# Performance work log

Measured on AMD Instinct MI355X. Metric: run time of the kernel, lower is better.

The kernel has to match this reference:

```python
import jax, jax.numpy as jnp
import numpy as np

NB = 8          # num_bins
HID = 128       # hidden channels of coupling ResidualNet
TB = 3.0        # tail_bound
MINB = 1e-3     # min bin width / height
MIND = 1e-3     # min derivative
DCONST = float(np.log(np.exp(1.0 - MIND) - 1.0))  # softplus(DCONST)+MIND == 1
LU_EPS = 1e-3


def rqs_inverse(x, uw, uh, ud):
    """Inverse monotonic rational-quadratic spline with linear tails (nflows math).
    x: [B,F]; uw,uh broadcastable to [B,F,NB]; ud broadcastable to [B,F,NB-1]."""
    K = NB
    uw = jnp.broadcast_to(uw, x.shape + (K,))
    uh = jnp.broadcast_to(uh, x.shape + (K,))
    ud = jnp.broadcast_to(ud, x.shape + (K - 1,))
    ud = jnp.pad(ud, [(0, 0)] * x.ndim + [(1, 1)], constant_values=DCONST)  # boundary derivs = 1
    inside = (x >= -TB) & (x <= TB)
    xi = jnp.clip(x, -TB, TB)

    def knots(u):
        v = MINB + (1.0 - MINB * K) * jax.nn.softmax(u, -1)
        c = jnp.concatenate([jnp.zeros(x.shape + (1,), x.dtype), jnp.cumsum(v, -1)], -1)
        c = 2.0 * TB * c - TB
        c = c.at[..., 0].set(-TB).at[..., -1].set(TB)
        return c, c[..., 1:] - c[..., :-1]

    cw, w = knots(uw)   # x-knots / bin widths
    ch, h = knots(uh)   # y-knots / bin heights
    d = MIND + jax.nn.softplus(ud)  # [B,F,K+1] knot derivatives

    # searchsorted on cumheights (inverse direction)
    locs = ch.at[..., -1].add(1e-6)
    idx = jnp.clip(jnp.sum((xi[..., None] >= locs).astype(jnp.int32), -1) - 1, 0, K - 1)[..., None]
    g = lambda a: jnp.take_along_axis(a, idx, -1)[..., 0]
    in_cw, in_w, in_ch, in_h = g(cw), g(w), g(ch), g(h)
    delta = in_h / in_w
    d0 = g(d)
    d1 = jnp.take_along_axis(d, idx + 1, -1)[..., 0]

    t = xi - in_ch
    s = d0 + d1 - 2.0 * delta
    a = t * s + in_h * (delta - d0)
    b = in_h * d0 - t * s
    c = -delta * t
    root = (2.0 * c) / (-b - jnp.sqrt(b * b - 4.0 * a * c))
    out = root * in_w + in_cw
    tm = root * (1.0 - root)
    den = delta + s * tm
    dnum = delta ** 2 * (d1 * root ** 2 + 2.0 * delta * tm + d0 * (1.0 - root) ** 2)
    ld = -(jnp.log(dnum) - 2.0 * jnp.log(den))
    return jnp.where(inside, out, x), jnp.where(inside, ld, 0.0)


def resnet(x, Wi, bi, Wb, bb, Wo, bo):
    # nflows ResidualNet: initial linear, 2 pre-activation residual blocks, final linear
    t = x @ Wi + bi
    for j in range(2):
        r = jax.nn.relu(t) @ Wb[2 * j] + bb[2 * j]
        r = jax.nn.relu(r) @ Wb[2 * j + 1] + bb[2 * j + 1]
        t = t + r
    return t @ Wo + bo


def coupling_inverse(z, Wi, bi, Wb, bb, Wo, bo, uw_u, uh_u, ud_u):
    # alternating mask: even dims = identity split, odd dims = transform split
    ident, trans = z[:, 0::2], z[:, 1::2]
    # unconditional spline on identity features is inverted FIRST, then feeds the net
    ident, ld_u = rqs_inverse(ident, uw_u, uh_u, ud_u)
    B, F = trans.shape
    p = resnet(ident, Wi, bi, Wb, bb, Wo, bo).reshape(B, F, 3 * NB - 1)
    scale = 1.0 / np.sqrt(HID)  # nflows divides widths/heights by sqrt(hidden_features)
    trans, ld_t = rqs_inverse(trans, p[..., :NB] * scale, p[..., NB:2 * NB] * scale, p[..., 2 * NB:])
    out = jnp.stack([ident, trans], -1).reshape(B, -1)
    return out, jnp.sum(ld_u, -1) + jnp.sum(ld_t, -1)


def log_prob(x, loc, log_scale, Wi, bi, Wb, bb, Wo, bo, uw_u, uh_u, ud_u,
             lu_lower, lu_upper, lu_ud, lu_b, perms):
    N, T, D = x.shape
    z = x.reshape(-1, D)
    lq = jnp.zeros((z.shape[0],), x.dtype)
    for i in (2, 1, 0):  # flows = [C0,LU0,C1,LU1,C2,LU2]; invert in reverse order
        # LULinearPermute.inverse: permute, then y = L(Ux) + b, logdet = sum log diag(U)
        zp = z[:, perms[i]]
        diag = jax.nn.softplus(lu_ud[i]) + LU_EPS
        U = jnp.triu(lu_upper[i], 1) + jnp.diag(diag)
        L = jnp.tril(lu_lower[i], -1) + jnp.eye(D, dtype=x.dtype)
        z = (zp @ U.T) @ L.T + lu_b[i]
        lq = lq + jnp.sum(jnp.log(diag))
        z, ld = coupling_inverse(z, Wi[i], bi[i], Wb[i], bb[i], Wo[i], bo[i],
                                 uw_u[i], uh_u[i], ud_u[i])
        lq = lq + ld
    # DiagGaussian base log-prob
    lq = lq - 0.5 * D * jnp.log(2.0 * jnp.pi) \
            - jnp.sum(log_scale + 0.5 * ((z - loc) / jnp.exp(log_scale)) ** 2, -1)
    return lq.reshape(N, T)


def setup_inputs():
    key = jax.random.key(0)
    ks = jax.random.split(key, 16)
    N, T, D, F = 8, 512, 550, 275
    OUT = F * (3 * NB - 1)
    s = 0.1
    return {
        "x": jax.random.normal(ks[0], (N, T, D), jnp.float32),
        "loc": 0.1 * jax.random.normal(ks[1], (D,), jnp.float32),
        "log_scale": jnp.zeros((D,), jnp.float32),
        "Wi": s * jax.random.normal(ks[2], (3, F, HID), jnp.float32),
        "bi": jnp.zeros((3, HID), jnp.float32),
        "Wb": s * jax.random.normal(ks[3], (3, 4, HID, HID), jnp.float32),
        "bb": jnp.zeros((3, 4, HID), jnp.float32),
        "Wo": 0.01 * jax.random.normal(ks[4], (3, HID, OUT), jnp.float32),
        "bo": 0.01 * jax.random.normal(ks[5], (3, OUT), jnp.float32),
        "uw_u": jax.random.uniform(ks[6], (3, F, NB), jnp.float32),
        "uh_u": jax.random.uniform(ks[7], (3, F, NB), jnp.float32),
        "ud_u": jax.random.uniform(ks[8], (3, F, NB - 1), jnp.float32),
        "lu_lower": 0.05 * jax.random.normal(ks[9], (3, D, D), jnp.float32),
        "lu_upper": 0.05 * jax.random.normal(ks[10], (3, D, D), jnp.float32),
        "lu_ud": jnp.full((3, D), DCONST, jnp.float32),
        "lu_b": jnp.zeros((3, D), jnp.float32),
        "perms": jnp.stack([jax.random.permutation(ks[11 + i], D) for i in range(3)]).astype(jnp.int32),
    }


def reference(x, loc, log_scale, Wi, bi, Wb, bb, Wo, bo, uw_u, uh_u, ud_u,
              lu_lower, lu_upper, lu_ud, lu_b, perms):
    # log_prob(x).reshape(N, T); calculate_likelihood would just apply exp/nan->0/clamp on top.
    return log_prob(x, loc, log_scale, Wi, bi, Wb, bb, Wo, bo, uw_u, uh_u, ud_u,
                    lu_lower, lu_upper, lu_ud, lu_b, perms)
```

## Files before the change

kernel.cpp:

```cpp
#include <hip/hip_runtime.h>


#define D_DIM 550
#define D_PAD 576
#define N_PAD_A 640
#define F_DIM 275
#define F_PAD 320
#define FP_HALF 288
#define HID_DIM 128
#define OUT_DIM 6325
#define OUT_PAD 6400
#define FT_PAD 276
#define WO24_ROWS (FT_PAD*24)
#define WO_GX (WO24_ROWS/48)
#define B_ROWS 4096
#define NBINS 8
#define TB_C 3.0f
#define MINB_C 0.001f
#define MIND_C 0.001f
#define DCONST_C 0.53974233f
#define LUEPS_C 0.001f
#define RSQRT_HID 0.08838834764831845f

typedef unsigned short ushort_t;
typedef __attribute__((ext_vector_type(8))) short short8;
typedef __attribute__((ext_vector_type(8))) unsigned short ushort8;
typedef __attribute__((ext_vector_type(4))) float f32x4;

__device__ __forceinline__ ushort_t f2bf(float f){
    union{float f; unsigned u;} v; v.f = f;
    unsigned r = v.u + 0x7fffu + ((v.u>>16)&1u);
    return (ushort_t)(r>>16);
}
__device__ __forceinline__ float bf2f(ushort_t h){
    union{unsigned u; float f;} v; v.u = ((unsigned)h)<<16;
    return v.f;
}
__device__ __forceinline__ float softplusf(float x){
    return fmaxf(x, 0.f) + __logf(1.f + __expf(-fabsf(x)));
}

__device__ __forceinline__ void knots_from_u(const float* u, float* c, float* w){
    float m = u[0];
#pragma unroll
    for(int k=1;k<NBINS;k++) m = fmaxf(m, u[k]);
    float e[NBINS]; float s = 0.f;
#pragma unroll
    for(int k=0;k<NBINS;k++){ e[k] = __expf(u[k]-m); s += e[k]; }
    float inv = 1.f/s;
    float cum = 0.f;
    c[0] = -TB_C;
#pragma unroll
    for(int k=0;k<NBINS;k++){
        float v = MINB_C + (1.f - MINB_C*(float)NBINS)*e[k]*inv;
        cum += v;
        c[k+1] = 2.f*TB_C*cum - TB_C;
    }
    c[NBINS] = TB_C;
#pragma unroll
    for(int k=0;k<NBINS;k++) w[k] = c[k+1]-c[k];
}

__device__ __forceinline__ void rqs_inv(float x,
                                        const float* cw, const float* w,
                                        const float* ch, const float* h,
                                        const float* d,
                                        float& out, float& ld){
    bool inside = (x >= -TB_C) && (x <= TB_C);
    float xi = fminf(fmaxf(x, -TB_C), TB_C);
    int idx = 0;
#pragma unroll
    for(int j=1;j<NBINS;j++) idx += (xi >= ch[j]) ? 1 : 0;
    float icw=cw[0], iw=w[0], ich=ch[0], ih=h[0], d0=d[0], d1=d[1];
#pragma unroll
    for(int j=1;j<NBINS;j++){
        if(idx==j){ icw=cw[j]; iw=w[j]; ich=ch[j]; ih=h[j]; d0=d[j]; d1=d[j+1]; }
    }
    float delta = ih/iw;
    float t  = xi - ich;
    float s  = d0 + d1 - 2.f*delta;
    float a  = t*s + ih*(delta - d0);
    float b  = ih*d0 - t*s;
    float c  = -delta*t;
    float disc = b*b - 4.f*a*c;
    float root = 2.f*c / (-b - sqrtf(fmaxf(disc, 0.f)));
    float o  = root*iw + icw;
    float tm = root*(1.f-root);
    float den  = delta + s*tm;
    float dnum = delta*delta*(d1*root*root + 2.f*delta*tm + d0*(1.f-root)*(1.f-root));
    float l = 2.f*__logf(den) - __logf(dnum);
    out = inside ? o : x;
    ld  = inside ? l : 0.f;
}

__global__ __launch_bounds__(256)
void fat_setup(const float* __restrict__ uw_u, const float* __restrict__ uh_u,
               const float* __restrict__ ud_u, float* __restrict__ knots,
               const float* __restrict__ lu_ud, float* __restrict__ logdiag,
               const float* __restrict__ bo, float* __restrict__ bo2,
               const float* __restrict__ x, ushort_t* __restrict__ xb,
               const float* __restrict__ lower, ushort_t* __restrict__ Lmb,
               float* __restrict__ lq, float* __restrict__ zbias,
               ushort_t* __restrict__ zOddT, ushort_t* __restrict__ Wo2){
    __shared__ float sm[4];
    int b = blockIdx.x, tid = threadIdx.x;
    if(b < 4){
        int g = b*256 + tid;
        if(g >= 3*F_DIM) return;
        float* kb = knots + (size_t)g*43;
        float c[9], w[8];
        knots_from_u(uw_u + (size_t)g*8, c, w);
#pragma unroll
        for(int k=0;k<9;k++) kb[k]=c[k];
#pragma unroll
        for(int k=0;k<8;k++) kb[9+k]=w[k];
        knots_from_u(uh_u + (size_t)g*8, c, w);
#pragma unroll
        for(int k=0;k<9;k++) kb[17+k]=c[k];
#pragma unroll
        for(int k=0;k<8;k++) kb[26+k]=w[k];
        float dend = MIND_C + softplusf(DCONST_C);
        kb[34]=dend; kb[42]=dend;
        const float* ud = ud_u + (size_t)g*7;
#pragma unroll
        for(int k=0;k<7;k++) kb[35+k] = MIND_C + softplusf(ud[k]);
    } else if(b < 5){
        float s = 0.f;
        for(int k=tid; k<3*D_DIM; k+=256) s += __logf(softplusf(lu_ud[k]) + LUEPS_C);
#pragma unroll
        for(int o=32;o>0;o>>=1) s += __shfl_down(s, o);
        if((tid&63)==0) sm[tid>>6]=s;
        __syncthreads();
        if(tid==0) logdiag[0] = sm[0]+sm[1]+sm[2]+sm[3];
    } else if(b < 80){
        int idx = (b-5)*256 + tid;
        if(idx >= 3*OUT_DIM) return;
        int l = idx/OUT_DIM, n = idx%OUT_DIM;
        int f = n/23, j = n - 23*f;
        bo2[(size_t)l*WO24_ROWS + f*24 + j] = bo[idx];
    } else if(b < 9296){
        int idx = (b-80)*256 + tid;
        if(idx >= B_ROWS*D_PAD) return;
        int r = idx / D_PAD, c = idx - r*D_PAD;
        float v = (r<B_ROWS && c<D_DIM) ? x[(size_t)r*D_DIM+c] : 0.f;
        xb[idx] = f2bf(v);
    } else if(b < 14246){
        int lb = b - 9296;
        int l = lb/1650;
        int rem = lb - l*1650;
        int j = rem/3;
        int xb3 = rem - j*3;
        int k = xb3*256 + tid;
        if(k >= D_DIM) return;
        const float* lw = lower + (size_t)l*D_DIM*D_DIM;
        ushort_t* Lp = Lmb + (size_t)l*N_PAD_A*D_PAD;
        float lv = (j>k) ? lw[(size_t)j*D_DIM+k] : (j==k ? 1.f : 0.f);
        Lp[(size_t)j*D_PAD+k] = f2bf(lv);
    } else if(b < 14262){
        int p = (b-14246)*256 + tid;
        if(p < B_ROWS) lq[p] = 0.f;
    } else if(b < 14265){
        int p = (b-14262)*256 + tid;
        if(p < D_PAD) zbias[p] = 0.f;
    } else if(b < 14369){
        int p = (b-14265)*256 + tid;
        if(p < 13*2048){
            int row = 275 + p/2048, ci = p%2048;
            ((unsigned*)zOddT)[(size_t)row*2048 + ci] = 0u;
        }
    } else if(b < 14594){
        int p = (b-14369)*256 + tid;
        if(p < 57408){
            int l = p/19136, r2 = p%19136;
            int rl = r2/64, ci = r2%64;
            int row = (rl<275) ? rl*24+23 : 6600+(rl-275);
            ((unsigned*)Wo2)[((size_t)l*WO24_ROWS + row)*64 + ci] = 0u;
        }
    } else {
        int p = (b-14594)*256 + tid;
        if(p < 897){
            int l = p/299, r = p%299;
            int idx2 = (r<275) ? r*24+23 : 6600+(r-275);
            bo2[(size_t)l*WO24_ROWS + idx2] = 0.f;
        }
    }
}

__device__ __forceinline__ void tc_body(const float* in, ushort_t* out,
                                        int K, int N, int Kpad, int Npad,
                                        long s_in, long s_out, int remap,
                                        int bx, int by, int bz,
                                        int tx, int ty, float (*t)[33]){
    in += (size_t)bz*s_in; out += (size_t)bz*s_out;
    int kb = bx*32, nb = by*32;
#pragma unroll
    for(int i=0;i<32;i+=8){
        int k = kb+ty+i, n = nb+tx;
        t[ty+i][tx] = (k<K && n<N) ? in[(size_t)k*N+n] : 0.f;
    }
    __syncthreads();
#pragma unroll
    for(int i=0;i<32;i+=8){
        int n = nb+ty+i, k = kb+tx;
        if(remap){
            if(n < OUT_DIM && k < Kpad){
                int f = n/23, j = n - 23*f;
                out[(size_t)(f*24+j)*Kpad+k] = f2bf(t[tx][ty+i]);
            }
        } else if(n<Npad && k<Kpad){
            out[(size_t)n*Kpad+k] = f2bf(t[tx][ty+i]);
        }
    }
}

__global__ __launch_bounds__(256)
void fat_trans(const float* __restrict__ Wi, ushort_t* __restrict__ WiT,
               const float* __restrict__ Wb, ushort_t* __restrict__ WbT,
               const float* __restrict__ Wo, ushort_t* __restrict__ Wo2,
               const float* __restrict__ upper, const float* __restrict__ ud,
               const int* __restrict__ perm, ushort_t* __restrict__ UpTb){
    __shared__ float t[32][33];
    int b = blockIdx.x, tid = threadIdx.x;
    int tx = tid & 31, ty = tid >> 5;
    if(b < 120){
        int z = b/40, rem = b%40, by = rem/10, bx = rem%10;
        tc_body(Wi, WiT, F_DIM, HID_DIM, F_PAD, HID_DIM,
                (long)F_DIM*HID_DIM, (long)F_PAD*HID_DIM, 0, bx, by, z, tx, ty, t);
    } else if(b < 312){
        int lb = b-120;
        int z = lb/16, rem = lb%16, by = rem/4, bx = rem%4;
        tc_body(Wb, WbT, HID_DIM, HID_DIM, HID_DIM, HID_DIM,
                (long)HID_DIM*HID_DIM, (long)HID_DIM*HID_DIM, 0, bx, by, z, tx, ty, t);
    } else if(b < 2712){
        int lb = b-312;
        int z = lb/800, rem = lb%800, by = rem/4, bx = rem%4;
        tc_body(Wo, Wo2, HID_DIM, OUT_DIM, HID_DIM, OUT_PAD,
                (long)HID_DIM*OUT_DIM, (long)WO24_ROWS*HID_DIM, 1, bx, by, z, tx, ty, t);
    } else {
        int lb = b-2712;
        int l = lb/324, rem = lb%324, by = rem/18, bx = rem%18;
        const float* up = upper + (size_t)l*D_DIM*D_DIM;
        const float* udl = ud + (size_t)l*D_DIM;
        const int* pm = perm + (size_t)l*D_DIM;
        ushort_t* Up = UpTb + (size_t)l*N_PAD_A*D_PAD;
        int j0 = bx*32, k0 = by*32;
#pragma unroll
        for(int i=0;i<32;i+=8){
            int j = j0+ty+i, k = k0+tx;
            float uv = 0.f;
            if(j<D_DIM && k<D_DIM){
                if(j<k)       uv = up[(size_t)j*D_DIM+k];
                else if(j==k) uv = softplusf(udl[k]) + LUEPS_C;
            }
            t[ty+i][tx] = uv;
        }
        __syncthreads();
#pragma unroll
        for(int i=0;i<32;i+=8){
            int k = k0+ty+i, j = j0+tx;
            if(k<D_DIM)
                Up[(size_t)pm[k]*D_PAD + j] = f2bf(t[tx][ty+i]);
        }
    }
}

template<int OUTBF>
__global__ __launch_bounds__(256)
void gemm_mfma(const ushort_t* __restrict__ A, const ushort_t* __restrict__ Bt,
               const float* __restrict__ bias, void* __restrict__ Cv,
               int M, int N, int Kpad, long sA, long sB, long sC){
    A  += (size_t)blockIdx.z*sA;
    Bt += (size_t)blockIdx.z*sB;
    __shared__ ushort_t As[128][72];
    __shared__ ushort_t Bs[128][72];
    int tid = threadIdx.x;
    int row0 = blockIdx.y*128, col0 = blockIdx.x*128;
    int wave = tid>>6, lane = tid&63;
    int wm = wave&1, wn = wave>>1;
    int lm = lane&15, quad = lane>>4;
    f32x4 acc[4][4] = {};
    for(int k0=0; k0<Kpad; k0+=64){
#pragma unroll
        for(int it=0; it<4; it++){
            int c = tid + it*256;
            int r = c>>3, c8 = (c&7)*8;
            *(ushort8*)&As[r][c8] = *(const ushort8*)(A + (size_t)(row0+r)*Kpad + k0 + c8);
            *(ushort8*)&Bs[r][c8] = *(const ushort8*)(Bt + (size_t)(col0+r)*Kpad + k0 + c8);
        }
        __syncthreads();
#pragma unroll
        for(int ks=0; ks<2; ks++){
            short8 af[4], bfr[4];
#pragma unroll
            for(int i=0;i<4;i++){
                af[i]  = *(const short8*)&As[wm*64 + i*16 + lm][ks*32 + quad*8];
                bfr[i] = *(const short8*)&Bs[wn*64 + i*16 + lm][ks*32 + quad*8];
            }
#pragma unroll
            for(int i=0;i<4;i++)
#pragma unroll
                for(int j=0;j<4;j++)
                    acc[i][j] = __builtin_amdgcn_mfma_f32_16x16x32_bf16(af[i], bfr[j], acc[i][j], 0, 0, 0);
        }
        __syncthreads();
    }
#pragma unroll
    for(int i=0;i<4;i++){
        int rbase = row0 + wm*64 + i*16 + quad*4;
#pragma unroll
        for(int j=0;j<4;j++){
            int gc = col0 + wn*64 + j*16 + lm;
            if(gc >= N) continue;
            float bv = bias[gc];
#pragma unroll
            for(int r=0;r<4;r++){
                int gr = rbase + r;
                float v = acc[i][j][r] + bv;
                if(OUTBF) ((ushort_t*)Cv + (size_t)blockIdx.z*sC)[(size_t)gr*N+gc] = f2bf(v);
                else      ((float*)Cv + (size_t)blockIdx.z*sC)[(size_t)gr*N+gc] = v;
            }
        }
    }
}

__global__ __launch_bounds__(256)
void resnet_fused(const ushort_t* __restrict__ identb,
                  const ushort_t* __restrict__ WiT,
                  const float* __restrict__ bi,
                  const ushort_t* __restrict__ WbT,
                  const float* __restrict__ bb,
                  ushort_t* __restrict__ tb){
    __shared__ ushort_t As2[16][136];
    int tid = threadIdx.x, wave = tid>>6, lane = tid&63;
    int lm = lane&15, quad = lane>>4;
    int r0 = blockIdx.x*16;
    int arow = r0 + lm;
    f32x4 cur[2] = {};
    f32x4 tsv[2];
    for(int k0=0; k0<F_PAD; k0+=64){
        const ushort_t* ap = identb + (size_t)arow*F_PAD + k0 + quad*8;
        short8 af0 = *(const short8*)(ap);
        short8 af1 = *(const short8*)(ap + 32);
#pragma unroll
        for(int jj=0;jj<2;jj++){
            int n = (wave*2+jj)*16 + lm;
            const ushort_t* wp = WiT + (size_t)n*F_PAD + k0 + quad*8;
            short8 b0 = *(const short8*)(wp);
            short8 b1 = *(const short8*)(wp + 32);
            cur[jj] = __builtin_amdgcn_mfma_f32_16x16x32_bf16(af0, b0, cur[jj], 0, 0, 0);
            cur[jj] = __builtin_amdgcn_mfma_f32_16x16x32_bf16(af1, b1, cur[jj], 0, 0, 0);
        }
    }
#pragma unroll
    for(int jj=0;jj<2;jj++){
        float bv = bi[(wave*2+jj)*16 + lm];
#pragma unroll
        for(int r=0;r<4;r++) cur[jj][r] += bv;
        tsv[jj] = cur[jj];
    }
    short8 wA[2][4], wB[2][4];
#pragma unroll
    for(int jj=0;jj<2;jj++){
        int n = (wave*2+jj)*16 + lm;
        const ushort_t* wp = WbT + (size_t)n*128 + quad*8;
#pragma unroll
        for(int ks=0;ks<4;ks++) wA[jj][ks] = *(const short8*)(wp + ks*32);
    }
#pragma unroll
    for(int st=0; st<4; st++){
        __syncthreads();
#pragma unroll
        for(int jj=0;jj<2;jj++)
#pragma unroll
            for(int r=0;r<4;r++)
                As2[quad*4 + r][(wave*2+jj)*16 + lm] = f2bf(fmaxf(cur[jj][r], 0.f));
        if(st < 3){
#pragma unroll
            for(int jj=0;jj<2;jj++){
                int n = (wave*2+jj)*16 + lm;
                const ushort_t* wp = WbT + (size_t)(st+1)*128*128 + (size_t)n*128 + quad*8;
#pragma unroll
                for(int ks=0;ks<4;ks++){
                    if(st & 1) wA[jj][ks] = *(const short8*)(wp + ks*32);
                    else       wB[jj][ks] = *(const short8*)(wp + ks*32);
                }
            }
        }
        __syncthreads();
        short8 af[4];
#pragma unroll
        for(int ks=0;ks<4;ks++) af[ks] = *(const short8*)&As2[lm][ks*32 + quad*8];
        f32x4 acc[2] = {};
#pragma unroll
        for(int ks=0;ks<4;ks++){
#pragma unroll
            for(int jj=0;jj<2;jj++){
                short8 bf = (st & 1) ? wB[jj][ks] : wA[jj][ks];
                acc[jj] = __builtin_amdgcn_mfma_f32_16x16x32_bf16(af[ks], bf, acc[jj], 0, 0, 0);
            }
        }
#pragma unroll
        for(int jj=0;jj<2;jj++){
            float bv = bb[st*128 + (wave*2+jj)*16 + lm];
#pragma unroll
            for(int r=0;r<4;r++) acc[jj][r] += bv;
        }
        if(st==1 || st==3){
#pragma unroll
            for(int jj=0;jj<2;jj++){
#pragma unroll
                for(int r=0;r<4;r++) acc[jj][r] += tsv[jj][r];
                tsv[jj] = acc[jj];
            }
        }
#pragma unroll
        for(int jj=0;jj<2;jj++) cur[jj] = acc[jj];
    }
#pragma unroll
    for(int jj=0;jj<2;jj++)
#pragma unroll
        for(int r=0;r<4;r++)
            tb[(size_t)(r0 + quad*4 + r)*HID_DIM + (wave*2+jj)*16 + lm] = f2bf(cur[jj][r]);
}

__global__ __launch_bounds__(320)
void zident(const float* __restrict__ z2, const float* __restrict__ knots,
            int layer, float* __restrict__ z2oddT,
            ushort_t* __restrict__ identb, float* __restrict__ lq){
    __shared__ float s[32][65];
    __shared__ float sm[5];
    int b = blockIdx.x, tid = threadIdx.x;
    if(b < 576){
        int r0 = (b & 63)*64, f0 = (b >> 6)*32;
        int f = tid & 31, rb = tid >> 5;
        if(tid < 256){
#pragma unroll
            for(int rr=0; rr<8; rr++){
                int r = rb + rr*8;
                int fg = f0 + f;
                float v = (fg < F_DIM) ? z2[(size_t)(r0+r)*D_DIM + 2*fg + 1] : 0.f;
                s[f][r] = v;
            }
        }
        __syncthreads();
        if(tid < 256){
            int lane = tid & 63, fb = tid >> 6;
#pragma unroll
            for(int ff=0; ff<8; ff++){
                int fo = fb + ff*4;
                z2oddT[(size_t)(f0+fo)*B_ROWS + r0 + lane] = s[fo][lane];
            }
        }
    } else {
        int row = b - 576;
        float ldv = 0.f;
        if(tid < F_DIM){
            const float* kb = knots + ((size_t)(layer*F_DIM + tid))*43;
            float x = z2[(size_t)row*D_DIM + 2*tid];
            float o, l;
            rqs_inv(x, kb, kb+9, kb+17, kb+26, kb+34, o, l);
            identb[(size_t)row*F_PAD + tid] = f2bf(o);
            ldv = l;
        } else {
            identb[(size_t)row*F_PAD + tid] = 0;
        }
        float v = ldv;
#pragma unroll
        for(int o=32;o>0;o>>=1) v += __shfl_down(v, o);
        if((tid&63)==0) sm[tid>>6]=v;
        __syncthreads();
        if(tid==0) lq[row] += sm[0]+sm[1]+sm[2]+sm[3]+sm[4];
    }
}

__global__ __launch_bounds__(256, 4)
void wo_spline(const ushort_t* __restrict__ tb,
               const ushort_t* __restrict__ Wo2,
               const float* __restrict__ bo2,
               const float* __restrict__ z2oddT,
               ushort_t* __restrict__ zOddT,
               float* __restrict__ ldpart){
    __shared__ __align__(16) char smem[128*51*4];
    __shared__ float ldred[128];
    ushort_t (*As)[72] = (ushort_t(*)[72])smem;
    ushort_t (*Bs)[72] = (ushort_t(*)[72])(smem + 128*72*2);
    float (*P)[51] = (float(*)[51])smem;
    int tid = threadIdx.x;
    int flat = blockIdx.y*WO_GX + blockIdx.x;
    int flat2 = (flat & 7)*(WO_GX*32/8) + (flat >> 3);
    int cbl = flat2 % WO_GX;
    int rbl = flat2 / WO_GX;
    int row0 = rbl*128, col0 = cbl*48;
    int wave = tid>>6, lane = tid&63;
    int lm = lane&15, quad = lane>>4;
    f32x4 acc[2][3] = {};
    for(int k0=0; k0<HID_DIM; k0+=64){
#pragma unroll
        for(int it=0; it<4; it++){
            int c = tid + it*256;
            int r = c>>3, c8 = (c&7)*8;
            *(ushort8*)&As[r][c8] = *(const ushort8*)(tb + (size_t)(row0+r)*HID_DIM + k0 + c8);
        }
#pragma unroll
        for(int it=0; it<2; it++){
            int v = tid + it*256;
            if(v < 384){
                int n = v>>3, c8 = (v&7)*8;
                *(ushort8*)&Bs[n][c8] = *(const ushort8*)(Wo2 + (size_t)(col0+n)*HID_DIM + k0 + c8);
            }
        }
        __syncthreads();
#pragma unroll
        for(int ks=0; ks<2; ks++){
            short8 af[2], bfr[3];
#pragma unroll
            for(int i=0;i<2;i++)
                af[i]  = *(const short8*)&As[wave*32 + i*16 + lm][ks*32 + quad*8];
#pragma unroll
            for(int j=0;j<3;j++)
                bfr[j] = *(const short8*)&Bs[j*16 + lm][ks*32 + quad*8];
#pragma unroll
            for(int i=0;i<2;i++)
#pragma unroll
                for(int j=0;j<3;j++)
                    acc[i][j] = __builtin_amdgcn_mfma_f32_16x16x32_bf16(af[i], bfr[j], acc[i][j], 0, 0, 0);
        }
        __syncthreads();
    }
#pragma unroll
    for(int j=0;j<3;j++){
        int cl = j*16 + lm;
        float bv = bo2[col0 + cl];
#pragma unroll
        for(int i=0;i<2;i++){
            int rl = wave*32 + i*16 + quad*4;
#pragma unroll
            for(int r=0;r<4;r++) P[rl+r][cl] = acc[i][j][r] + bv;
        }
    }
    __syncthreads();
    int row = tid & 127, feat = tid >> 7;
    int fg = cbl*2 + feat;
    float ldsum = 0.f;
    const float dend = MIND_C + softplusf(DCONST_C);
    if(fg < F_DIM){
        const float* q = &P[row][feat*24];
        float xv = z2oddT[(size_t)fg*B_ROWS + row0 + row];
        bool inside = (xv >= -TB_C) && (xv <= TB_C);
        float xi = fminf(fmaxf(xv, -TB_C), TB_C);
        float eh[8];
        float mh = -1e30f, sh = 0.f;
#pragma unroll
        for(int k=0;k<8;k++){ float u = q[8+k]*RSQRT_HID; eh[k]=u; mh=fmaxf(mh,u); }
#pragma unroll
        for(int k=0;k<8;k++){ eh[k] = __expf(eh[k]-mh); sh += eh[k]; }
        float invh = (1.f - MINB_C*8.f)/sh;
        int idx = 0;
        {
            float cum = 0.f;
#pragma unroll
            for(int k=0;k<7;k++){
                cum += MINB_C + eh[k]*invh;
                float ck = 2.f*TB_C*cum - TB_C;
                idx += (xi >= ck) ? 1 : 0;
            }
        }
        float ich = -TB_C, ihh = 0.f;
        {
            float cum = 0.f, cprev = -TB_C;
#pragma unroll
            for(int k=0;k<8;k++){
                cum += MINB_C + eh[k]*invh;
                float ck = (k==7) ? TB_C : (2.f*TB_C*cum - TB_C);
                if(idx==k){ ich = cprev; ihh = ck - cprev; }
                cprev = ck;
            }
        }
        float ew[8];
        float mw = -1e30f, sw = 0.f;
#pragma unroll
        for(int k=0;k<8;k++){ float u = q[k]*RSQRT_HID; ew[k]=u; mw=fmaxf(mw,u); }
#pragma unroll
        for(int k=0;k<8;k++){ ew[k] = __expf(ew[k]-mw); sw += ew[k]; }
        float invw = (1.f - MINB_C*8.f)/sw;
        float icw = -TB_C, iww = 0.f;
        {
            float cum = 0.f, cprev = -TB_C;
#pragma unroll
            for(int k=0;k<8;k++){
                cum += MINB_C + ew[k]*invw;
                float ck = (k==7) ? TB_C : (2.f*TB_C*cum - TB_C);
                if(idx==k){ icw = cprev; iww = ck - cprev; }
                cprev = ck;
            }
        }
        float d0 = (idx==0) ? dend : (MIND_C + softplusf(q[15+idx]));
        float d1 = (idx==7) ? dend : (MIND_C + softplusf(q[16+idx]));
        float delta = ihh/iww;
        float t  = xi - ich;
        float s  = d0 + d1 - 2.f*delta;
        float a  = t*s + ihh*(delta - d0);
        float b  = ihh*d0 - t*s;
        float c  = -delta*t;
        float disc = fmaxf(b*b - 4.f*a*c, 0.f);
        float root = 2.f*c / (-b - sqrtf(disc));
        float o  = root*iww + icw;
        float tm = root*(1.f-root);
        float den  = delta + s*tm;
        float dnum = delta*delta*(d1*root*root + 2.f*delta*tm + d0*(1.f-root)*(1.f-root));
        float l = 2.f*__logf(den) - __logf(dnum);
        zOddT[(size_t)fg*B_ROWS + row0 + row] = f2bf(inside ? o : xv);
        ldsum = inside ? l : 0.f;
    }
    if(tid >= 128) ldred[tid-128] = ldsum;
    __syncthreads();
    if(tid < 128) ldpart[(size_t)cbl*B_ROWS + row0 + tid] = ldsum + ldred[tid];
}

__global__ __launch_bounds__(256)
void interleave_z(const ushort_t* __restrict__ identb,
                  const ushort_t* __restrict__ zOddT,
                  const float* __restrict__ ldpart,
                  ushort_t* __restrict__ znb,
                  float* __restrict__ lq){
    __shared__ ushort_t s[FP_HALF][34];
    int r0 = blockIdx.x*32;
    int tid = threadIdx.x;
#pragma unroll
    for(int i=0;i<36;i++){
        int idx = tid + i*256;
        int f = idx>>5, r = idx&31;
        s[f][r] = zOddT[(size_t)f*B_ROWS + r0 + r];
    }
    __syncthreads();
    int wv = tid>>6, lane = tid&63;
#pragma unroll
    for(int k=0;k<8;k++){
        int r = wv + k*4;
        const ushort_t* idr = identb + (size_t)(r0+r)*F_PAD;
        unsigned* orow = (unsigned*)(znb + (size_t)(r0+r)*D_PAD);
#pragma unroll
        for(int c=0;c<5;c++){
            int f = lane + c*64;
            if(f < FP_HALF){
                unsigned lo = idr[f];
                unsigned hi = s[f][r];
                orow[f] = lo | (hi<<16);
            }
        }
    }
    if(tid < 32){
        float acc = 0.f;
        for(int cb=0; cb<WO_GX; cb++)
            acc += ldpart[(size_t)cb*B_ROWS + r0 + tid];
        lq[r0 + tid] += acc;
    }
}


__global__ __launch_bounds__(320)
void finalize_kernel(const ushort_t* __restrict__ zb, const float* __restrict__ loc,
                     const float* __restrict__ lsc, const float* __restrict__ lq,
                     const float* __restrict__ logdiag, float* __restrict__ out){
    int row = blockIdx.x; int tid = threadIdx.x;
    float s = 0.f;
    for(int k=tid; k<D_DIM; k+=320){
        float l = lsc[k];
        float diff = (bf2f(zb[(size_t)row*D_PAD+k])-loc[k])*__expf(-l);
        s += l + 0.5f*diff*diff;
    }
    __shared__ float sm[5];
#pragma unroll
    for(int o=32;o>0;o>>=1) s += __shfl_down(s, o);
    if((tid&63)==0) sm[tid>>6]=s;
    __syncthreads();
    if(tid==0){
        float tot = sm[0]+sm[1]+sm[2]+sm[3]+sm[4];
        out[row] = lq[row] + logdiag[0] - 275.f*1.8378770664f - tot;
    }
}


extern "C" void kernel_launch(void* const* d_in, const int* in_sizes, int n_in,
                              void* d_out, int out_size, void* d_ws, size_t ws_size,
                              hipStream_t stream){
    const float* x        = (const float*)d_in[0];
    const float* loc      = (const float*)d_in[1];
    const float* lsc      = (const float*)d_in[2];
    const float* Wi       = (const float*)d_in[3];
    const float* bi       = (const float*)d_in[4];
    const float* Wb       = (const float*)d_in[5];
    const float* bb       = (const float*)d_in[6];
    const float* Wo       = (const float*)d_in[7];
    const float* bo       = (const float*)d_in[8];
    const float* uw_u     = (const float*)d_in[9];
    const float* uh_u     = (const float*)d_in[10];
    const float* ud_u     = (const float*)d_in[11];
    const float* lu_lower = (const float*)d_in[12];
    const float* lu_upper = (const float*)d_in[13];
    const float* lu_ud    = (const float*)d_in[14];
    const float* lu_b     = (const float*)d_in[15];
    const int*   perms    = (const int*)d_in[16];
    float* out = (float*)d_out;

    char* base = (char*)d_ws;
    size_t off = 0;
    auto alloc = [&](size_t bytes)->char*{
        char* p = base + off;
        off += (bytes + 255) & ~(size_t)255;
        return p;
    };
    float* lq      = (float*)alloc(B_ROWS*4);
    float* zbias   = (float*)alloc(D_PAD*4);
    float* logdiag = (float*)alloc(64*4);
    float* knots   = (float*)alloc((size_t)3*F_DIM*43*4);
    float* z2      = (float*)alloc((size_t)B_ROWS*D_DIM*4);
    float* z2oddT  = (float*)alloc((size_t)FP_HALF*B_ROWS*4);
    float* ldpart  = (float*)alloc((size_t)WO_GX*B_ROWS*4);
    float* bo2     = (float*)alloc((size_t)3*WO24_ROWS*4);
    ushort_t* xb   = (ushort_t*)alloc((size_t)B_ROWS*D_PAD*2);
    ushort_t* zbf0 = (ushort_t*)alloc((size_t)B_ROWS*D_PAD*2);
    ushort_t* zbf1 = (ushort_t*)alloc((size_t)B_ROWS*D_PAD*2);
    ushort_t* zOddT= (ushort_t*)alloc((size_t)FP_HALF*B_ROWS*2);
    ushort_t* Lmb  = (ushort_t*)alloc((size_t)3*N_PAD_A*D_PAD*2);
    ushort_t* UpTb = (ushort_t*)alloc((size_t)3*N_PAD_A*D_PAD*2);
    ushort_t* Apb  = (ushort_t*)alloc((size_t)3*N_PAD_A*D_PAD*2);
    ushort_t* identb=(ushort_t*)alloc((size_t)B_ROWS*F_PAD*2);
    ushort_t* tb   = (ushort_t*)alloc((size_t)B_ROWS*HID_DIM*2);
    ushort_t* WiT  = (ushort_t*)alloc((size_t)3*HID_DIM*F_PAD*2);
    ushort_t* WbT  = (ushort_t*)alloc((size_t)3*4*HID_DIM*HID_DIM*2);
    ushort_t* Wo2  = (ushort_t*)alloc((size_t)3*WO24_ROWS*HID_DIM*2);

    hipMemsetAsync(Lmb, 0, (size_t)3*N_PAD_A*D_PAD*2, stream);
    hipMemsetAsync(UpTb, 0, (size_t)3*N_PAD_A*D_PAD*2, stream);

    fat_setup<<<dim3(14598), dim3(256), 0, stream>>>(
        uw_u, uh_u, ud_u, knots, lu_ud, logdiag, bo, bo2,
        x, xb, lu_lower, Lmb, lq, zbias, zOddT, Wo2);

    fat_trans<<<dim3(3684), dim3(256), 0, stream>>>(
        Wi, WiT, Wb, WbT, Wo, Wo2, lu_upper, lu_ud, perms, UpTb);

    gemm_mfma<1><<<dim3(5, 5, 3), dim3(256), 0, stream>>>(
        Lmb, UpTb, zbias, Apb, N_PAD_A, D_PAD, D_PAD,
        (long)N_PAD_A*D_PAD, (long)N_PAD_A*D_PAD, (long)N_PAD_A*D_PAD);

    const ushort_t* zcur_b = xb;
    ushort_t* zbf[2] = {zbf0, zbf1};
    int zi = 0;

    for(int it=0; it<3; ++it){
        int i = 2 - it;

        gemm_mfma<0><<<dim3(N_PAD_A/128, B_ROWS/128), dim3(256), 0, stream>>>(
            zcur_b, Apb + (size_t)i*N_PAD_A*D_PAD, lu_b + (size_t)i*D_DIM,
            z2, B_ROWS, D_DIM, D_PAD, 0, 0, 0);

        zident<<<dim3(576 + B_ROWS), dim3(320), 0, stream>>>(
            z2, knots, i, z2oddT, identb, lq);

        resnet_fused<<<dim3(B_ROWS/16), dim3(256), 0, stream>>>(
            identb, WiT + (size_t)i*HID_DIM*F_PAD, bi + (size_t)i*HID_DIM,
            WbT + (size_t)i*4*HID_DIM*HID_DIM, bb + (size_t)i*4*HID_DIM, tb);

        wo_spline<<<dim3(WO_GX, B_ROWS/128), dim3(256), 0, stream>>>(
            tb, Wo2 + (size_t)i*WO24_ROWS*HID_DIM, bo2 + (size_t)i*WO24_ROWS,
            z2oddT, zOddT, ldpart);

        interleave_z<<<dim3(B_ROWS/32), dim3(256), 0, stream>>>(
            identb, zOddT, ldpart, zbf[zi], lq);

        zcur_b = zbf[zi];
        zi ^= 1;
    }

    finalize_kernel<<<dim3(B_ROWS), dim3(320), 0, stream>>>(
        zcur_b, loc, lsc, lq, logdiag, out);
}
```

Baseline: 372.5 us.

## Merge setup/transpose kernels, replace memsets with pad zeroing, fuse finalize

Merges the weight-transpose kernel into the setup kernel and replaces the two full-buffer memsets of the LU factor matrices with targeted zeroing of only their padding regions. The final interleave pass is specialised to compute the Gaussian base log-prob directly from the identity and spline halves and write the output, so the separate finalize kernel and the last interleaved bf16 write are dropped. This cuts launch count and memory traffic. The pad-zeroing blocks and the Lmb/UpTb fill blocks now run in the same launch on disjoint regions, which relies on the offset arithmetic being exact.

```diff
diff --git a/kernel.cpp b/kernel.cpp
--- a/kernel.cpp
+++ b/kernel.cpp
@@ -21,6 +21,11 @@
 #define DCONST_C 0.53974233f
 #define LUEPS_C 0.001f
 #define RSQRT_HID 0.08838834764831845f
+#define LU_U32_PER_LAYER 184320
+#define PAD_STRIP 7150
+#define PAD_PER_LAYER 33070
+#define PAD_TOTAL 99210
+#define PAD_BLOCKS 388
 
 typedef unsigned short ushort_t;
 typedef __attribute__((ext_vector_type(8))) short short8;
@@ -93,6 +98,33 @@
     ld  = inside ? l : 0.f;
 }
 
+__device__ __forceinline__ void tc_body(const float* in, ushort_t* out,
+                                        int K, int N, int Kpad, int Npad,
+                                        long s_in, long s_out, int remap,
+                                        int bx, int by, int bz,
+                                        int tx, int ty, float (*t)[33]){
+    in += (size_t)bz*s_in; out += (size_t)bz*s_out;
+    int kb = bx*32, nb = by*32;
+#pragma unroll
+    for(int i=0;i<32;i+=8){
+        int k = kb+ty+i, n = nb+tx;
+        t[ty+i][tx] = (k<K && n<N) ? in[(size_t)k*N+n] : 0.f;
+    }
+    __syncthreads();
+#pragma unroll
+    for(int i=0;i<32;i+=8){
+        int n = nb+ty+i, k = kb+tx;
+        if(remap){
+            if(n < OUT_DIM && k < Kpad){
+                int f = n/23, j = n - 23*f;
+                out[(size_t)(f*24+j)*Kpad+k] = f2bf(t[tx][ty+i]);
+            }
+        } else if(n<Npad && k<Kpad){
+            out[(size_t)n*Kpad+k] = f2bf(t[tx][ty+i]);
+        }
+    }
+}
+
 __global__ __launch_bounds__(256)
 void fat_setup(const float* __restrict__ uw_u, const float* __restrict__ uh_u,
                const float* __restrict__ ud_u, float* __restrict__ knots,
@@ -101,9 +133,16 @@
                const float* __restrict__ x, ushort_t* __restrict__ xb,
                const float* __restrict__ lower, ushort_t* __restrict__ Lmb,
                float* __restrict__ lq, float* __restrict__ zbias,
-               ushort_t* __restrict__ zOddT, ushort_t* __restrict__ Wo2){
+               ushort_t* __restrict__ zOddT, ushort_t* __restrict__ Wo2,
+               const float* __restrict__ Wi, ushort_t* __restrict__ WiT,
+               const float* __restrict__ Wb, ushort_t* __restrict__ WbT,
+               const float* __restrict__ Wo,
+               const float* __restrict__ upper, const int* __restrict__ perm,
+               ushort_t* __restrict__ UpTb){
     __shared__ float sm[4];
+    __shared__ float t[32][33];
     int b = blockIdx.x, tid = threadIdx.x;
+    int tx = tid & 31, ty = tid >> 5;
     if(b < 4){
         int g = b*256 + tid;
         if(g >= 3*F_DIM) return;
@@ -176,71 +215,51 @@
             int row = (rl<275) ? rl*24+23 : 6600+(rl-275);
             ((unsigned*)Wo2)[((size_t)l*WO24_ROWS + row)*64 + ci] = 0u;
         }
-    } else {
+    } else if(b < 14598){
         int p = (b-14594)*256 + tid;
         if(p < 897){
             int l = p/299, r = p%299;
             int idx2 = (r<275) ? r*24+23 : 6600+(r-275);
             bo2[(size_t)l*WO24_ROWS + idx2] = 0.f;
         }
-    }
-}
-
-__device__ __forceinline__ void tc_body(const float* in, ushort_t* out,
-                                        int K, int N, int Kpad, int Npad,
-                                        long s_in, long s_out, int remap,
-                                        int bx, int by, int bz,
-                                        int tx, int ty, float (*t)[33]){
-    in += (size_t)bz*s_in; out += (size_t)bz*s_out;
-    int kb = bx*32, nb = by*32;
-#pragma unroll
-    for(int i=0;i<32;i+=8){
-        int k = kb+ty+i, n = nb+tx;
-        t[ty+i][tx] = (k<K && n<N) ? in[(size_t)k*N+n] : 0.f;
-    }
-    __syncthreads();
-#pragma unroll
-    for(int i=0;i<32;i+=8){
-        int n = nb+ty+i, k = kb+tx;
-        if(remap){
-            if(n < OUT_DIM && k < Kpad){
-                int f = n/23, j = n - 23*f;
-                out[(size_t)(f*24+j)*Kpad+k] = f2bf(t[tx][ty+i]);
-            }
-        } else if(n<Npad && k<Kpad){
-            out[(size_t)n*Kpad+k] = f2bf(t[tx][ty+i]);
-        }
-    }
-}
-
-__global__ __launch_bounds__(256)
-void fat_trans(const float* __restrict__ Wi, ushort_t* __restrict__ WiT,
-               const float* __restrict__ Wb, ushort_t* __restrict__ WbT,
-               const float* __restrict__ Wo, ushort_t* __restrict__ Wo2,
-               const float* __restrict__ upper, const float* __restrict__ ud,
-               const int* __restrict__ perm, ushort_t* __restrict__ UpTb){
-    __shared__ float t[32][33];
-    int b = blockIdx.x, tid = threadIdx.x;
-    int tx = tid & 31, ty = tid >> 5;
-    if(b < 120){
-        int z = b/40, rem = b%40, by = rem/10, bx = rem%10;
+    } else if(b < 14986){
+        int p = (b-14598)*256 + tid;
+        if(p < PAD_TOTAL){
+            int l = p/PAD_PER_LAYER, r = p%PAD_PER_LAYER;
+            unsigned off;
+            if(r < PAD_STRIP){ int j = r/13, ci = r%13; off = j*288u + 275u + ci; }
+            else { int r2 = r-PAD_STRIP; int row = 550 + r2/288, ci = r2%288; off = row*288u + ci; }
+            ((unsigned*)Lmb)[(size_t)l*LU_U32_PER_LAYER + off] = 0u;
+        }
+    } else if(b < 15374){
+        int p = (b-14986)*256 + tid;
+        if(p < PAD_TOTAL){
+            int l = p/PAD_PER_LAYER, r = p%PAD_PER_LAYER;
+            unsigned off;
+            if(r < PAD_STRIP){ int j = r/13, ci = r%13; off = j*288u + 275u + ci; }
+            else { int r2 = r-PAD_STRIP; int row = 550 + r2/288, ci = r2%288; off = row*288u + ci; }
+            ((unsigned*)UpTb)[(size_t)l*LU_U32_PER_LAYER + off] = 0u;
+        }
+    } else if(b < 15494){
+        int lb = b-15374;
+        int z = lb/40, rem = lb%40, by = rem/10, bx = rem%10;
         tc_body(Wi, WiT, F_DIM, HID_DIM, F_PAD, HID_DIM,
                 (long)F_DIM*HID_DIM, (long)F_PAD*HID_DIM, 0, bx, by, z, tx, ty, t);
-    } else if(b < 312){
-        int lb = b-120;
+    } else if(b < 15686){
+        int lb = b-15494;
         int z = lb/16, rem = lb%16, by = rem/4, bx = rem%4;
         tc_body(Wb, WbT, HID_DIM, HID_DIM, HID_DIM, HID_DIM,
                 (long)HID_DIM*HID_DIM, (long)HID_DIM*HID_DIM, 0, bx, by, z, tx, ty, t);
-    } else if(b < 2712){
-        int lb = b-312;
+    } else if(b < 18086){
+        int lb = b-15686;
         int z = lb/800, rem = lb%800, by = rem/4, bx = rem%4;
         tc_body(Wo, Wo2, HID_DIM, OUT_DIM, HID_DIM, OUT_PAD,
                 (long)HID_DIM*OUT_DIM, (long)WO24_ROWS*HID_DIM, 1, bx, by, z, tx, ty, t);
     } else {
-        int lb = b-2712;
+        int lb = b-18086;
         int l = lb/324, rem = lb%324, by = rem/18, bx = rem%18;
         const float* up = upper + (size_t)l*D_DIM*D_DIM;
-        const float* udl = ud + (size_t)l*D_DIM;
+        const float* udl = lu_ud + (size_t)l*D_DIM;
         const int* pm = perm + (size_t)l*D_DIM;
         ushort_t* Up = UpTb + (size_t)l*N_PAD_A*D_PAD;
         int j0 = bx*32, k0 = by*32;
@@ -617,13 +636,19 @@
     if(tid < 128) ldpart[(size_t)cbl*B_ROWS + row0 + tid] = ldsum + ldred[tid];
 }
 
+template<int LAST>
 __global__ __launch_bounds__(256)
 void interleave_z(const ushort_t* __restrict__ identb,
                   const ushort_t* __restrict__ zOddT,
                   const float* __restrict__ ldpart,
                   ushort_t* __restrict__ znb,
-                  float* __restrict__ lq){
+                  float* __restrict__ lq,
+                  const float* __restrict__ loc,
+                  const float* __restrict__ lsc,
+                  const float* __restrict__ logdiag,
+                  float* __restrict__ out){
     __shared__ ushort_t s[FP_HALF][34];
+    __shared__ float lqv[32];
     int r0 = blockIdx.x*32;
     int tid = threadIdx.x;
 #pragma unroll
@@ -633,50 +658,47 @@
         s[f][r] = zOddT[(size_t)f*B_ROWS + r0 + r];
     }
     __syncthreads();
-    int wv = tid>>6, lane = tid&63;
-#pragma unroll
-    for(int k=0;k<8;k++){
-        int r = wv + k*4;
-        const ushort_t* idr = identb + (size_t)(r0+r)*F_PAD;
-        unsigned* orow = (unsigned*)(znb + (size_t)(r0+r)*D_PAD);
-#pragma unroll
-        for(int c=0;c<5;c++){
-            int f = lane + c*64;
-            if(f < FP_HALF){
-                unsigned lo = idr[f];
-                unsigned hi = s[f][r];
-                orow[f] = lo | (hi<<16);
-            }
-        }
-    }
     if(tid < 32){
         float acc = 0.f;
         for(int cb=0; cb<WO_GX; cb++)
             acc += ldpart[(size_t)cb*B_ROWS + r0 + tid];
-        lq[r0 + tid] += acc;
-    }
-}
-
-
-__global__ __launch_bounds__(320)
-void finalize_kernel(const ushort_t* __restrict__ zb, const float* __restrict__ loc,
-                     const float* __restrict__ lsc, const float* __restrict__ lq,
-                     const float* __restrict__ logdiag, float* __restrict__ out){
-    int row = blockIdx.x; int tid = threadIdx.x;
-    float s = 0.f;
-    for(int k=tid; k<D_DIM; k+=320){
-        float l = lsc[k];
-        float diff = (bf2f(zb[(size_t)row*D_PAD+k])-loc[k])*__expf(-l);
-        s += l + 0.5f*diff*diff;
-    }
-    __shared__ float sm[5];
-#pragma unroll
-    for(int o=32;o>0;o>>=1) s += __shfl_down(s, o);
-    if((tid&63)==0) sm[tid>>6]=s;
-    __syncthreads();
-    if(tid==0){
-        float tot = sm[0]+sm[1]+sm[2]+sm[3]+sm[4];
-        out[row] = lq[row] + logdiag[0] - 275.f*1.8378770664f - tot;
+        if(LAST) lqv[tid] = lq[r0 + tid] + acc;
+        else     lq[r0 + tid] += acc;
+    }
+    if(LAST) __syncthreads();
+    int wv = tid>>6, lane = tid&63;
+#pragma unroll
+    for(int k=0;k<8;k++){
+        int r = wv + k*4;
+        const ushort_t* idr = identb + (size_t)(r0+r)*F_PAD;
+        if(!LAST){
+            unsigned* orow = (unsigned*)(znb + (size_t)(r0+r)*D_PAD);
+#pragma unroll
+            for(int c=0;c<5;c++){
+                int f = lane + c*64;
+                if(f < FP_HALF){
+                    unsigned lo = idr[f];
+                    unsigned hi = s[f][r];
+                    orow[f] = lo | (hi<<16);
+                }
+            }
+        } else {
+            float fsum = 0.f;
+#pragma unroll
+            for(int c=0;c<5;c++){
+                int f = lane + c*64;
+                if(f < F_DIM){
+                    float le = lsc[2*f], lo2 = lsc[2*f+1];
+                    float de = (bf2f(idr[f])  - loc[2*f])  *__expf(-le);
+                    float dо = (bf2f(s[f][r]) - loc[2*f+1])*__expf(-lo2);
+                    fsum += le + 0.5f*de*de + lo2 + 0.5f*dо*dо;
+                }
+            }
+#pragma unroll
+            for(int o=32;o>0;o>>=1) fsum += __shfl_down(fsum, o);
+            if(lane==0)
+                out[r0+r] = lqv[r] + logdiag[0] - 275.f*1.8378770664f - fsum;
+        }
     }
 }
 
@@ -731,15 +753,10 @@
     ushort_t* WbT  = (ushort_t*)alloc((size_t)3*4*HID_DIM*HID_DIM*2);
     ushort_t* Wo2  = (ushort_t*)alloc((size_t)3*WO24_ROWS*HID_DIM*2);
 
-    hipMemsetAsync(Lmb, 0, (size_t)3*N_PAD_A*D_PAD*2, stream);
-    hipMemsetAsync(UpTb, 0, (size_t)3*N_PAD_A*D_PAD*2, stream);
-
-    fat_setup<<<dim3(14598), dim3(256), 0, stream>>>(
+    fat_setup<<<dim3(19058), dim3(256), 0, stream>>>(
         uw_u, uh_u, ud_u, knots, lu_ud, logdiag, bo, bo2,
-        x, xb, lu_lower, Lmb, lq, zbias, zOddT, Wo2);
-
-    fat_trans<<<dim3(3684), dim3(256), 0, stream>>>(
-        Wi, WiT, Wb, WbT, Wo, Wo2, lu_upper, lu_ud, perms, UpTb);
+        x, xb, lu_lower, Lmb, lq, zbias, zOddT, Wo2,
+        Wi, WiT, Wb, WbT, Wo, lu_upper, perms, UpTb);
 
     gemm_mfma<1><<<dim3(5, 5, 3), dim3(256), 0, stream>>>(
         Lmb, UpTb, zbias, Apb, N_PAD_A, D_PAD, D_PAD,
@@ -767,13 +784,17 @@
             tb, Wo2 + (size_t)i*WO24_ROWS*HID_DIM, bo2 + (size_t)i*WO24_ROWS,
             z2oddT, zOddT, ldpart);
 
-        interleave_z<<<dim3(B_ROWS/32), dim3(256), 0, stream>>>(
-            identb, zOddT, ldpart, zbf[zi], lq);
+        if(it < 2){
+            interleave_z<0><<<dim3(B_ROWS/32), dim3(256), 0, stream>>>(
+                identb, zOddT, ldpart, zbf[zi], lq,
+                nullptr, nullptr, nullptr, nullptr);
+        } else {
+            interleave_z<1><<<dim3(B_ROWS/32), dim3(256), 0, stream>>>(
+                identb, zOddT, ldpart, zbf[zi], lq,
+                loc, lsc, logdiag, out);
+        }
 
         zcur_b = zbf[zi];
         zi ^= 1;
     }
-
-    finalize_kernel<<<dim3(B_ROWS), dim3(320), 0, stream>>>(
-        zcur_b, loc, lsc, lq, logdiag, out);
-}
+}
```

Result: faster. 363.7 us (-2.3%).
